# Optimization experiments

Hardware: AMD Instinct MI355X
Metric: run time of the kernel (lower is better)

## Reference

```python
import jax, jax.numpy as jnp
import numpy as np

L, H, NH, DH, FF, V, S, B = 12, 768, 12, 64, 3072, 21128, 512, 8
SEP = 102
LN_EPS = 1e-12


def _ln(x, g, b):
    m = jnp.mean(x, axis=-1, keepdims=True)
    v = jnp.mean(jnp.square(x - m), axis=-1, keepdims=True)
    return (x - m) * jax.lax.rsqrt(v + LN_EPS) * g + b


def setup_inputs() -> dict:
    key = jax.random.key(0)
    ctr = [0]
    def nk():
        ctr[0] += 1
        return jax.random.fold_in(key, ctr[0])
    def p(shape):
        return (0.02 * jax.random.normal(nk(), shape)).astype(jnp.float32)

    input_ids = jax.random.randint(nk(), (B, S), 0, V)
    sep_cols = jax.random.randint(nk(), (B,), 32, 128)
    input_ids = input_ids.at[jnp.arange(B), sep_cols].set(SEP)  # plant [SEP] per row
    labels = jax.random.randint(nk(), (B, S), 0, V)

    return dict(
        input_ids=input_ids, labels=labels,
        word_emb=p((V, H)), pos_emb=p((S, H)), type_emb=p((2, H)),
        emb_ln_g=jnp.ones((H,), jnp.float32), emb_ln_b=jnp.zeros((H,), jnp.float32),
        Wq=p((L, H, H)), bq=jnp.zeros((L, H), jnp.float32),
        Wk=p((L, H, H)), bk=jnp.zeros((L, H), jnp.float32),
        Wv=p((L, H, H)), bv=jnp.zeros((L, H), jnp.float32),
        Wo=p((L, H, H)), bo=jnp.zeros((L, H), jnp.float32),
        ln1_g=jnp.ones((L, H), jnp.float32), ln1_b=jnp.zeros((L, H), jnp.float32),
        Wi=p((L, H, FF)), bi=jnp.zeros((L, FF), jnp.float32),
        Wd=p((L, FF, H)), bd=jnp.zeros((L, H), jnp.float32),
        ln2_g=jnp.ones((L, H), jnp.float32), ln2_b=jnp.zeros((L, H), jnp.float32),
        Wc=p((H, V)), bc=jnp.zeros((V,), jnp.float32),
    )


def reference(input_ids, labels, word_emb, pos_emb, type_emb, emb_ln_g, emb_ln_b,
              Wq, bq, Wk, bk, Wv, bv, Wo, bo, ln1_g, ln1_b,
              Wi, bi, Wd, bd, ln2_g, ln2_b, Wc, bc):
    Bn, Sn = input_ids.shape
    # UniLM prefix-causal mask: bidirectional up to (and incl.) first SEP, causal after
    eq = input_ids == SEP
    sep = jnp.where(eq.any(axis=1), jnp.argmax(eq, axis=1), Sn - 1)        # [B]
    qi = jnp.arange(Sn)[:, None]
    ki = jnp.arange(Sn)[None, :]
    causal = (ki <= qi)                                                    # [S,S]
    prefix = (qi[None] <= sep[:, None, None]) & (ki[None] <= sep[:, None, None])
    mask = (causal[None] | prefix).astype(jnp.float32)                     # [B,S,S]
    bias = ((1.0 - mask) * -1e4)[:, None]                                  # [B,1,S,S]

    # BERT embeddings (token_type all zeros)
    x = word_emb[input_ids] + pos_emb[None, :Sn] + type_emb[0]
    x = _ln(x, emb_ln_g, emb_ln_b)

    scale = 1.0 / np.sqrt(DH).astype(np.float32)
    for l in range(L):
        q = (x @ Wq[l] + bq[l]).reshape(Bn, Sn, NH, DH)
        k = (x @ Wk[l] + bk[l]).reshape(Bn, Sn, NH, DH)
        v = (x @ Wv[l] + bv[l]).reshape(Bn, Sn, NH, DH)
        scores = jnp.einsum('bqhd,bkhd->bhqk', q, k) * scale + bias        # [B,NH,S,S]
        probs = jax.nn.softmax(scores, axis=-1)
        ctx = jnp.einsum('bhqk,bkhd->bqhd', probs, v).reshape(Bn, Sn, H)
        x = _ln(x + ctx @ Wo[l] + bo[l], ln1_g[l], ln1_b[l])
        h = jax.nn.gelu(x @ Wi[l] + bi[l], approximate=False)
        x = _ln(x + h @ Wd[l] + bd[l], ln2_g[l], ln2_b[l])

    logits = x @ Wc + bc                                                   # [B,S,V]
    logp = jax.nn.log_softmax(logits, axis=-1)
    valid = labels >= 0                                                    # ignore_index=-100
    safe = jnp.where(valid, labels, 0)
    nll = -jnp.take_along_axis(logp, safe[..., None], axis=-1)[..., 0]
    loss = jnp.sum(nll * valid) / jnp.maximum(jnp.sum(valid), 1)
    return loss
```

## Files before the change

### kernel.cpp

```cpp
#include <hip/hip_runtime.h>
#include <hip/hip_bf16.h>
#include <cmath>

namespace {

constexpr int LAYERS = 12;
constexpr int H   = 768;
constexpr int NH  = 12;
constexpr int DH  = 64;
constexpr int FF  = 3072;
constexpr int V   = 21128;
constexpr int S   = 512;
constexpr int B   = 8;
constexpr int M   = B * S;
constexpr int SEP = 102;
constexpr int NPAD = 21248;
constexpr int NT64 = NPAD / 64;
constexpr int QKVN = 3 * H;
constexpr size_t MHc = (size_t)M * H;

typedef __attribute__((ext_vector_type(8))) short short8;
typedef __attribute__((ext_vector_type(4))) float floatx4;

__device__ __forceinline__ float geluf(float x) {
  return 0.5f * x * (1.0f + erff(x * 0.70710678118654752f));
}

__device__ __forceinline__ void gload16(const void* g, void* l) {
  __builtin_amdgcn_global_load_lds(
      (const __attribute__((address_space(1))) void*)g,
      (__attribute__((address_space(3))) void*)l, 16, 0, 0);
}

__device__ __forceinline__ unsigned short f2bf(float f) {
  __hip_bfloat16 h = __float2bfloat16(f);
  return *reinterpret_cast<unsigned short*>(&h);
}

__device__ __forceinline__ float block_sum256(float v, float* red) {
  int tid = threadIdx.x;
  red[tid] = v; __syncthreads();
  for (int s2 = 128; s2 > 0; s2 >>= 1) {
    if (tid < s2) red[tid] += red[tid + s2];
    __syncthreads();
  }
  float r = red[0];
  __syncthreads();
  return r;
}

__device__ __forceinline__ float block_max256(float v, float* red) {
  int tid = threadIdx.x;
  red[tid] = v; __syncthreads();
  for (int s2 = 128; s2 > 0; s2 >>= 1) {
    if (tid < s2) red[tid] = fmaxf(red[tid], red[tid + s2]);
    __syncthreads();
  }
  float r = red[0];
  __syncthreads();
  return r;
}

__global__ void sep_kernel(const int* __restrict__ ids, int* __restrict__ sep) {
  int b = blockIdx.x;
  __shared__ int red[256];
  int m = S - 1;
  for (int s = threadIdx.x; s < S; s += 256)
    if (ids[b * S + s] == SEP) m = min(m, s);
  red[threadIdx.x] = m; __syncthreads();
  for (int s2 = 128; s2 > 0; s2 >>= 1) {
    if (threadIdx.x < s2) red[threadIdx.x] = min(red[threadIdx.x], red[threadIdx.x + s2]);
    __syncthreads();
  }
  if (threadIdx.x == 0) sep[b] = red[0];
}

__global__ __launch_bounds__(256) void transpose_kernel(
    const float* __restrict__ W, __hip_bfloat16* __restrict__ Wt,
    int K, int N, int Npad, size_t in_stride, size_t out_stride) {
  const float* Wz = W + (size_t)blockIdx.z * in_stride;
  __hip_bfloat16* Wtz = Wt + (size_t)blockIdx.z * out_stride;
  __shared__ float tile[32][33];
  int k0 = blockIdx.x * 32, n0 = blockIdx.y * 32;
  int tx = threadIdx.x & 31, ty = threadIdx.x >> 5;
  #pragma unroll
  for (int i = 0; i < 4; i++) {
    int kk = k0 + ty + i * 8, nn = n0 + tx;
    tile[ty + i * 8][tx] = (kk < K && nn < N) ? Wz[(size_t)kk * N + nn] : 0.f;
  }
  __syncthreads();
  #pragma unroll
  for (int i = 0; i < 4; i++) {
    int nn = n0 + ty + i * 8, kk = k0 + tx;
    if (nn < Npad && kk < K)
      Wtz[(size_t)nn * K + kk] = __float2bfloat16(tile[tx][ty + i * 8]);
  }
}

__global__ __launch_bounds__(256) void embed_kernel(
    const int* __restrict__ ids, const float* __restrict__ we,
    const float* __restrict__ pe, const float* __restrict__ te,
    const float* __restrict__ g, const float* __restrict__ bta,
    float* __restrict__ x, __hip_bfloat16* __restrict__ xb) {
  __shared__ float red[256];
  int tok = blockIdx.x;
  int s = tok % S;
  int id = ids[tok];
  float vals[3];
  #pragma unroll
  for (int i = 0; i < 3; i++) {
    int hh = threadIdx.x + i * 256;
    vals[i] = we[(size_t)id * H + hh] + pe[(size_t)s * H + hh] + te[hh];
  }
  float mean = block_sum256(vals[0] + vals[1] + vals[2], red) * (1.0f / H);
  float sq = 0.f;
  #pragma unroll
  for (int i = 0; i < 3; i++) { float d = vals[i] - mean; sq += d * d; }
  float var = block_sum256(sq, red) * (1.0f / H);
  float inv = rsqrtf(var + 1e-12f);
  #pragma unroll
  for (int i = 0; i < 3; i++) {
    int hh = threadIdx.x + i * 256;
    float o = (vals[i] - mean) * inv * g[hh] + bta[hh];
    x[(size_t)tok * H + hh] = o;
    xb[(size_t)tok * H + hh] = __float2bfloat16(o);
  }
}

template <int NS>
__global__ __launch_bounds__(256) void add_ln_kernel(
    const float* __restrict__ resid, const float* __restrict__ t,
    const float* __restrict__ g, const float* __restrict__ bta,
    float* __restrict__ out, __hip_bfloat16* __restrict__ outb) {
  __shared__ float red[256];
  int tok = blockIdx.x;
  float vals[3];
  #pragma unroll
  for (int i = 0; i < 3; i++) {
    size_t idx = (size_t)tok * H + threadIdx.x + i * 256;
    float v = resid[idx];
    #pragma unroll
    for (int z = 0; z < NS; z++) v += t[z * MHc + idx];
    vals[i] = v;
  }
  float mean = block_sum256(vals[0] + vals[1] + vals[2], red) * (1.0f / H);
  float sq = 0.f;
  #pragma unroll
  for (int i = 0; i < 3; i++) { float d = vals[i] - mean; sq += d * d; }
  float var = block_sum256(sq, red) * (1.0f / H);
  float inv = rsqrtf(var + 1e-12f);
  #pragma unroll
  for (int i = 0; i < 3; i++) {
    int hh = threadIdx.x + i * 256;
    float o = (vals[i] - mean) * inv * g[hh] + bta[hh];
    out[(size_t)tok * H + hh] = o;
    outb[(size_t)tok * H + hh] = __float2bfloat16(o);
  }
}

template <int K, int N, int EPI, int SPLIT = 1>
__global__ __launch_bounds__(256) void mfma_gemm(
    const short* __restrict__ A, const short* __restrict__ Bt,
    const float* __restrict__ bias,
    float* __restrict__ Cf, __hip_bfloat16* __restrict__ Cb,
    const int* __restrict__ labels, float2* __restrict__ partials,
    float* __restrict__ lablogit,
    __hip_bfloat16* __restrict__ Cb2, __hip_bfloat16* __restrict__ Cb3,
    const float* __restrict__ bias2, const float* __restrict__ bias3) {
  __shared__ __align__(16) short lds_a[128 * 32];
  __shared__ __align__(16) short lds_b[128 * 32];
  const int tid = threadIdx.x, lane = tid & 63, w = tid >> 6;
  const int wm = w >> 1, wn = w & 1;
  const int row0 = blockIdx.y * 128, col0 = blockIdx.x * 128;
  const int g = lane >> 4, c16 = lane & 15;
  const int srow = w * 32 + (lane >> 2);
  const int schunk = lane & 3;
  floatx4 acc[4][4] = {};

  constexpr int Ks = K / SPLIT;
  const int koff = (SPLIT > 1) ? (int)blockIdx.z * Ks : 0;

  for (int k0 = koff; k0 < koff + Ks; k0 += 32) {
    #pragma unroll
    for (int j = 0; j < 2; j++) {
      int m = srow + j * 16;
      int cg = schunk ^ ((m >> 1) & 3);
      gload16(A + (size_t)(row0 + m) * K + (k0 + cg * 8), lds_a + w * 1024 + j * 512);
      gload16(Bt + (size_t)(col0 + m) * K + (k0 + cg * 8), lds_b + w * 1024 + j * 512);
    }
    __syncthreads();
    short8 af[4], bfr[4];
    #pragma unroll
    for (int t = 0; t < 4; t++) {
      int rm = wm * 64 + t * 16 + c16;
      af[t] = *(const short8*)(lds_a + rm * 32 + ((g ^ ((rm >> 1) & 3)) << 3));
      int rn = wn * 64 + t * 16 + c16;
      bfr[t] = *(const short8*)(lds_b + rn * 32 + ((g ^ ((rn >> 1) & 3)) << 3));
    }
    #pragma unroll
    for (int mt = 0; mt < 4; mt++)
      #pragma unroll
      for (int nt = 0; nt < 4; nt++)
        acc[mt][nt] = __builtin_amdgcn_mfma_f32_16x16x32_bf16(af[mt], bfr[nt], acc[mt][nt], 0, 0, 0);
    __syncthreads();
  }

  if constexpr (EPI == 0) {
    float* Cfz = Cf + (size_t)blockIdx.z * ((size_t)M * N);
    #pragma unroll
    for (int mt = 0; mt < 4; mt++)
      #pragma unroll
      for (int r = 0; r < 4; r++) {
        int row = row0 + wm * 64 + mt * 16 + g * 4 + r;
        #pragma unroll
        for (int nt = 0; nt < 4; nt++) {
          int col = col0 + wn * 64 + nt * 16 + c16;
          float bb = (SPLIT == 1 || blockIdx.z == 0) ? bias[col] : 0.f;
          Cfz[(size_t)row * N + col] = acc[mt][nt][r] + bb;
        }
      }
  } else if constexpr (EPI == 1 || EPI == 2) {
    #pragma unroll
    for (int mt = 0; mt < 4; mt++)
      #pragma unroll
      for (int r = 0; r < 4; r++) {
        int row = row0 + wm * 64 + mt * 16 + g * 4 + r;
        #pragma unroll
        for (int nt = 0; nt < 4; nt++) {
          int col = col0 + wn * 64 + nt * 16 + c16;
          float vv = acc[mt][nt][r] + bias[col];
          if constexpr (EPI == 2) vv = geluf(vv);
          Cb[(size_t)row * N + col] = __float2bfloat16(vv);
        }
      }
  } else if constexpr (EPI == 4) {
    unsigned short* vt = (unsigned short*)Cb;
    #pragma unroll
    for (int mt = 0; mt < 4; mt++) {
      int row = row0 + wm * 64 + mt * 16 + g * 4;
      int bb = row >> 9, s0 = row & 511;
      #pragma unroll
      for (int nt = 0; nt < 4; nt++) {
        int col = col0 + wn * 64 + nt * 16 + c16;
        int h = col >> 6, d = col & 63;
        float bcol = bias[col];
        uint2 u;
        unsigned short p0 = f2bf(acc[mt][nt][0] + bcol);
        unsigned short p1 = f2bf(acc[mt][nt][1] + bcol);
        unsigned short p2 = f2bf(acc[mt][nt][2] + bcol);
        unsigned short p3 = f2bf(acc[mt][nt][3] + bcol);
        u.x = (unsigned int)p0 | ((unsigned int)p1 << 16);
        u.y = (unsigned int)p2 | ((unsigned int)p3 << 16);
        *(uint2*)(vt + ((size_t)((bb * NH + h) * DH + d) << 9) + s0) = u;
      }
    }
  } else if constexpr (EPI == 5) {
    const int sect = col0 / H;
    const int lc0 = col0 - sect * H;
    if (sect < 2) {
      __hip_bfloat16* out = (sect == 0) ? Cb : Cb2;
      const float* bptr = (sect == 0) ? bias : bias2;
      #pragma unroll
      for (int mt = 0; mt < 4; mt++)
        #pragma unroll
        for (int r = 0; r < 4; r++) {
          int row = row0 + wm * 64 + mt * 16 + g * 4 + r;
          #pragma unroll
          for (int nt = 0; nt < 4; nt++) {
            int lc = lc0 + wn * 64 + nt * 16 + c16;
            out[(size_t)row * H + lc] = __float2bfloat16(acc[mt][nt][r] + bptr[lc]);
          }
        }
    } else {
      unsigned short* vt = (unsigned short*)Cb3;
      #pragma unroll
      for (int mt = 0; mt < 4; mt++) {
        int row = row0 + wm * 64 + mt * 16 + g * 4;
        int bb = row >> 9, s0 = row & 511;
        #pragma unroll
        for (int nt = 0; nt < 4; nt++) {
          int lc = lc0 + wn * 64 + nt * 16 + c16;
          int h = lc >> 6, d = lc & 63;
          float bcol = bias3[lc];
          uint2 u;
          unsigned short p0 = f2bf(acc[mt][nt][0] + bcol);
          unsigned short p1 = f2bf(acc[mt][nt][1] + bcol);
          unsigned short p2 = f2bf(acc[mt][nt][2] + bcol);
          unsigned short p3 = f2bf(acc[mt][nt][3] + bcol);
          u.x = (unsigned int)p0 | ((unsigned int)p1 << 16);
          u.y = (unsigned int)p2 | ((unsigned int)p3 << 16);
          *(uint2*)(vt + ((size_t)((bb * NH + h) * DH + d) << 9) + s0) = u;
        }
      }
    }
  } else {
    #pragma unroll
    for (int mt = 0; mt < 4; mt++)
      #pragma unroll
      for (int r = 0; r < 4; r++) {
        int row = row0 + wm * 64 + mt * 16 + g * 4 + r;
        int lab = labels[row];
        float vals[4];
        float rmax = -1e30f;
        #pragma unroll
        for (int nt = 0; nt < 4; nt++) {
          int col = col0 + wn * 64 + nt * 16 + c16;
          float vv = (col < V) ? (acc[mt][nt][r] + bias[col]) : -60000.0f;
          vals[nt] = vv;
          rmax = fmaxf(rmax, vv);
          if (col == lab) lablogit[row] = vv;
        }
        #pragma unroll
        for (int d = 1; d < 16; d <<= 1) rmax = fmaxf(rmax, __shfl_xor(rmax, d, 64));
        float se = 0.f;
        #pragma unroll
        for (int nt = 0; nt < 4; nt++) se += __expf(vals[nt] - rmax);
        #pragma unroll
        for (int d = 1; d < 16; d <<= 1) se += __shfl_xor(se, d, 64);
        if (c16 == 0)
          partials[(size_t)row * NT64 + (col0 >> 6) + wn] = make_float2(rmax, se);
      }
  }
}

__global__ __launch_bounds__(256) void flash_attn(
    const short* __restrict__ q, const short* __restrict__ k,
    const short* __restrict__ vt, const int* __restrict__ sep,
    __hip_bfloat16* __restrict__ ctx) {
  constexpr int KT = 128;
  __shared__ __align__(16) short Qs[64 * 64];
  __shared__ __align__(16) short Ks[128 * 64];
  __shared__ __align__(16) short Vts[64 * 128];
  __shared__ __align__(16) short Pb[64 * 136];
  __shared__ __align__(16) float wm4[4][64];
  __shared__ __align__(16) float wl4[4][64];
  __shared__ __align__(16) float m_run[64], l_run[64], alpha_s[64], mnew_s[64];

  const int tid = threadIdx.x, lane = tid & 63, w = tid >> 6;
  const int g = lane >> 4, c16 = lane & 15;
  const int qt0 = blockIdx.x * 64, h = blockIdx.y, b = blockIdx.z;
  const int sepb = sep[b];

  if (tid < 64) { m_run[tid] = -1e30f; l_run[tid] = 0.f; }

  #pragma unroll
  for (int t = 0; t < 2; t++) {
    int id = (w * 2 + t) * 64 + lane;
    int row = id >> 3, slot = id & 7;
    int c = slot ^ (row & 7);
    gload16(q + (size_t)(b * S + qt0 + row) * H + h * DH + c * 8,
            Qs + (w * 2 + t) * 512);
  }

  int niter = (qt0 + 64 + KT - 1) / KT;
  int sepit = (sepb >> 7) + 1;
  if (sepit > niter) niter = sepit;

  floatx4 accO[4] = {};
  short8 qf[4][2];

  for (int it = 0; it < niter; ++it) {
    int kk0 = it * KT;
    __syncthreads();
    #pragma unroll
    for (int t = 0; t < 4; t++) {
      int id = (w * 4 + t) * 64 + lane;
      {
        int row = id >> 3, slot = id & 7, c = slot ^ (row & 7);
        gload16(k + (size_t)(b * S + kk0 + row) * H + h * DH + c * 8,
                Ks + (w * 4 + t) * 512);
      }
      {
        int row = id >> 4, slot = id & 15, c = slot ^ (row & 15);
        gload16(vt + (size_t)((b * NH + h) * DH + row) * S + kk0 + c * 8,
                Vts + (w * 4 + t) * 512);
      }
    }
    __syncthreads();

    if (it == 0) {
      #pragma unroll
      for (int nt = 0; nt < 4; nt++)
        #pragma unroll
        for (int st = 0; st < 2; st++) {
          int qq = nt * 16 + c16;
          int slot = (st * 4 + g) ^ (qq & 7);
          qf[nt][st] = *(const short8*)(Qs + qq * 64 + slot * 8);
        }
    }

    floatx4 accS[2][4] = {};
    #pragma unroll
    for (int st = 0; st < 2; st++) {
      short8 af[2];
      #pragma unroll
      for (int mt = 0; mt < 2; mt++) {
        int kkr = w * 32 + mt * 16 + c16;
        int slot = (st * 4 + g) ^ (kkr & 7);
        af[mt] = *(const short8*)(Ks + kkr * 64 + slot * 8);
      }
      #pragma unroll
      for (int mt = 0; mt < 2; mt++)
        #pragma unroll
        for (int nt = 0; nt < 4; nt++)
          accS[mt][nt] = __builtin_amdgcn_mfma_f32_16x16x32_bf16(
              af[mt], qf[nt][st], accS[mt][nt], 0, 0, 0);
    }

    float sc[2][4][4];
    float pm[4] = {-1e30f, -1e30f, -1e30f, -1e30f};
    #pragma unroll
    for (int mt = 0; mt < 2; mt++)
      #pragma unroll
      for (int nt = 0; nt < 4; nt++)
        #pragma unroll
        for (int r = 0; r < 4; r++) {
          int kkg = kk0 + w * 32 + mt * 16 + g * 4 + r;
          int qg = qt0 + nt * 16 + c16;
          bool allowed = (kkg <= qg) || (qg <= sepb && kkg <= sepb);
          float vv = accS[mt][nt][r] * 0.125f + (allowed ? 0.f : -1e4f);
          sc[mt][nt][r] = vv;
          pm[nt] = fmaxf(pm[nt], vv);
        }
    #pragma unroll
    for (int nt = 0; nt < 4; nt++) {
      pm[nt] = fmaxf(pm[nt], __shfl_xor(pm[nt], 16, 64));
      pm[nt] = fmaxf(pm[nt], __shfl_xor(pm[nt], 32, 64));
    }
    if (lane < 16) {
      #pragma unroll
      for (int nt = 0; nt < 4; nt++) wm4[w][nt * 16 + c16] = pm[nt];
    }
    __syncthreads();
    if (tid < 64) {
      float mit = fmaxf(fmaxf(wm4[0][tid], wm4[1][tid]), fmaxf(wm4[2][tid], wm4[3][tid]));
      float mold = m_run[tid];
      float mnew = fmaxf(mold, mit);
      float al = __expf(mold - mnew);
      m_run[tid] = mnew;
      alpha_s[tid] = al;
      mnew_s[tid] = mnew;
      l_run[tid] *= al;
    }
    __syncthreads();

    float psum[4] = {};
    #pragma unroll
    for (int mt = 0; mt < 2; mt++)
      #pragma unroll
      for (int nt = 0; nt < 4; nt++) {
        int qg = nt * 16 + c16;
        float mn = mnew_s[qg];
        unsigned short pk[4];
        #pragma unroll
        for (int r = 0; r < 4; r++) {
          float p = __expf(sc[mt][nt][r] - mn);
          psum[nt] += p;
          pk[r] = f2bf(p);
        }
        int kb = w * 32 + mt * 16 + g * 4;
        uint2 u;
        u.x = (unsigned int)pk[0] | ((unsigned int)pk[1] << 16);
        u.y = (unsigned int)pk[2] | ((unsigned int)pk[3] << 16);
        *(uint2*)(Pb + qg * 136 + kb) = u;
      }
    #pragma unroll
    for (int nt = 0; nt < 4; nt++) {
      psum[nt] += __shfl_xor(psum[nt], 16, 64);
      psum[nt] += __shfl_xor(psum[nt], 32, 64);
    }
    if (lane < 16) {
      #pragma unroll
      for (int nt = 0; nt < 4; nt++) wl4[w][nt * 16 + c16] = psum[nt];
    }
    {
      float4 a4 = *(const float4*)(alpha_s + w * 16 + g * 4);
      #pragma unroll
      for (int nt = 0; nt < 4; nt++) {
        accO[nt][0] *= a4.x; accO[nt][1] *= a4.y;
        accO[nt][2] *= a4.z; accO[nt][3] *= a4.w;
      }
    }
    __syncthreads();
    if (tid < 64)
      l_run[tid] += wl4[0][tid] + wl4[1][tid] + wl4[2][tid] + wl4[3][tid];

    #pragma unroll
    for (int st = 0; st < 4; st++) {
      short8 pf = *(const short8*)(Pb + (w * 16 + c16) * 136 + st * 32 + g * 8);
      #pragma unroll
      for (int nt = 0; nt < 4; nt++) {
        int d = nt * 16 + c16;
        int slot = (st * 4 + g) ^ (d & 15);
        short8 vf = *(const short8*)(Vts + d * 128 + slot * 8);
        accO[nt] = __builtin_amdgcn_mfma_f32_16x16x32_bf16(pf, vf, accO[nt], 0, 0, 0);
      }
    }
  }

  __syncthreads();
  float4 lv = *(const float4*)(l_run + w * 16 + g * 4);
  float linv[4] = {1.0f / lv.x, 1.0f / lv.y, 1.0f / lv.z, 1.0f / lv.w};
  #pragma unroll
  for (int r = 0; r < 4; r++) {
    int row = b * S + qt0 + w * 16 + g * 4 + r;
    #pragma unroll
    for (int nt = 0; nt < 4; nt++)
      ctx[(size_t)row * H + h * DH + nt * 16 + c16] =
          __float2bfloat16(accO[nt][r] * linv[r]);
  }
}

__global__ __launch_bounds__(256) void loss_kernel(
    const float2* __restrict__ partials, const float* __restrict__ lablogit,
    const int* __restrict__ labels, float* __restrict__ acc) {
  int tok = blockIdx.x;
  if (labels[tok] < 0) return;
  __shared__ float red[256];
  float lm = -1e30f;
  for (int t = threadIdx.x; t < NT64; t += 256)
    lm = fmaxf(lm, partials[(size_t)tok * NT64 + t].x);
  float Mx = block_max256(lm, red);
  float ls = 0.f;
  for (int t = threadIdx.x; t < NT64; t += 256) {
    float2 p = partials[(size_t)tok * NT64 + t];
    ls += p.y * __expf(p.x - Mx);
  }
  float Ssum = block_sum256(ls, red);
  if (threadIdx.x == 0) {
    float nll = (Mx + logf(Ssum)) - lablogit[tok];
    atomicAdd(&acc[0], nll);
    atomicAdd(&acc[1], 1.0f);
  }
}

__global__ void finalize_kernel(const float* __restrict__ acc, float* __restrict__ out) {
  out[0] = acc[0] / fmaxf(acc[1], 1.0f);
}

}

extern "C" void kernel_launch(void* const* d_in, const int* in_sizes, int n_in,
                              void* d_out, int out_size, void* d_ws, size_t ws_size,
                              hipStream_t stream) {
  const int*   input_ids = (const int*)d_in[0];
  const int*   labels    = (const int*)d_in[1];
  const float* word_emb  = (const float*)d_in[2];
  const float* pos_emb   = (const float*)d_in[3];
  const float* type_emb  = (const float*)d_in[4];
  const float* emb_ln_g  = (const float*)d_in[5];
  const float* emb_ln_b  = (const float*)d_in[6];
  const float* Wq = (const float*)d_in[7];
  const float* bq = (const float*)d_in[8];
  const float* Wk = (const float*)d_in[9];
  const float* bk = (const float*)d_in[10];
  const float* Wv = (const float*)d_in[11];
  const float* bv = (const float*)d_in[12];
  const float* Wo = (const float*)d_in[13];
  const float* bo = (const float*)d_in[14];
  const float* ln1_g = (const float*)d_in[15];
  const float* ln1_b = (const float*)d_in[16];
  const float* Wi = (const float*)d_in[17];
  const float* bi = (const float*)d_in[18];
  const float* Wd = (const float*)d_in[19];
  const float* bd = (const float*)d_in[20];
  const float* ln2_g = (const float*)d_in[21];
  const float* ln2_b = (const float*)d_in[22];
  const float* Wc = (const float*)d_in[23];
  const float* bc = (const float*)d_in[24];

  char* base = (char*)d_ws;
  size_t off = 0;
  auto alloc = [&](size_t bytes) -> void* {
    void* p = base + off;
    off = (off + bytes + 255) & ~(size_t)255;
    return p;
  };
  const size_t MH = (size_t)M * H;
  float*          x        = (float*)alloc(MH * 4);
  float*          t2       = (float*)alloc(MH * 4 * 4);
  __hip_bfloat16* xb       = (__hip_bfloat16*)alloc(MH * 2);
  __hip_bfloat16* qb       = (__hip_bfloat16*)alloc(MH * 2);
  __hip_bfloat16* kb       = (__hip_bfloat16*)alloc(MH * 2);
  __hip_bfloat16* vt       = (__hip_bfloat16*)alloc((size_t)B * NH * DH * S * 2);
  __hip_bfloat16* ctxb     = (__hip_bfloat16*)alloc(MH * 2);
  __hip_bfloat16* t1b      = (__hip_bfloat16*)alloc((size_t)M * FF * 2);
  float2*         partials = (float2*)alloc((size_t)M * NT64 * 8);
  float*          lablogit = (float*)alloc((size_t)M * 4);
  float*          acc      = (float*)alloc(2 * 4);
  int*            sep      = (int*)alloc(B * 4);
  __hip_bfloat16* wqkv_t = (__hip_bfloat16*)alloc((size_t)LAYERS * QKVN * H * 2);
  __hip_bfloat16* wo_t = (__hip_bfloat16*)alloc((size_t)LAYERS * H * H * 2);
  __hip_bfloat16* wi_t = (__hip_bfloat16*)alloc((size_t)FF * H * 2);
  __hip_bfloat16* wd_t = (__hip_bfloat16*)alloc((size_t)H * FF * 2);
  __hip_bfloat16* wc_t = (__hip_bfloat16*)alloc((size_t)NPAD * H * 2);

  hipMemsetAsync(acc, 0, 2 * sizeof(float), stream);

  sep_kernel<<<B, 256, 0, stream>>>(input_ids, sep);
  embed_kernel<<<M, 256, 0, stream>>>(input_ids, word_emb, pos_emb, type_emb,
                                      emb_ln_g, emb_ln_b, x, xb);

  {
    dim3 tg(H / 32, H / 32, LAYERS);
    transpose_kernel<<<tg, 256, 0, stream>>>(Wq, wqkv_t, H, H, H,
                                             (size_t)H * H, (size_t)QKVN * H);
    transpose_kernel<<<tg, 256, 0, stream>>>(Wk, wqkv_t + (size_t)H * H, H, H, H,
                                             (size_t)H * H, (size_t)QKVN * H);
    transpose_kernel<<<tg, 256, 0, stream>>>(Wv, wqkv_t + (size_t)2 * H * H, H, H, H,
                                             (size_t)H * H, (size_t)QKVN * H);
    transpose_kernel<<<tg, 256, 0, stream>>>(Wo, wo_t, H, H, H, (size_t)H * H, (size_t)H * H);
    dim3 tgc(H / 32, NPAD / 32, 1);
    transpose_kernel<<<tgc, 256, 0, stream>>>(Wc, wc_t, H, V, NPAD, 0, 0);
  }

  dim3 gQKV(QKVN / 128, M / 128);
  dim3 gO(H / 128, M / 128, 2);
  dim3 gF(FF / 128, M / 128);
  dim3 gD(H / 128, M / 128, 4);
  dim3 gAttn(S / 64, NH, B);

  for (int l = 0; l < LAYERS; l++) {
    transpose_kernel<<<dim3(H / 32, FF / 32, 1), 256, 0, stream>>>(
        Wi + (size_t)l * H * FF, wi_t, H, FF, FF, 0, 0);
    transpose_kernel<<<dim3(FF / 32, H / 32, 1), 256, 0, stream>>>(
        Wd + (size_t)l * FF * H, wd_t, FF, H, H, 0, 0);

    const short* xbs = (const short*)xb;
    mfma_gemm<H, QKVN, 5><<<gQKV, 256, 0, stream>>>(
        xbs, (const short*)(wqkv_t + (size_t)l * QKVN * H), bq + (size_t)l * H,
        nullptr, qb, nullptr, nullptr, nullptr,
        kb, vt, bk + (size_t)l * H, bv + (size_t)l * H);
    flash_attn<<<gAttn, 256, 0, stream>>>(
        (const short*)qb, (const short*)kb, (const short*)vt, sep, ctxb);
    mfma_gemm<H, H, 0, 2><<<gO, 256, 0, stream>>>(
        (const short*)ctxb, (const short*)(wo_t + (size_t)l * H * H), bo + (size_t)l * H,
        t2, nullptr, nullptr, nullptr, nullptr,
        nullptr, nullptr, nullptr, nullptr);
    add_ln_kernel<2><<<M, 256, 0, stream>>>(x, t2, ln1_g + (size_t)l * H,
                                            ln1_b + (size_t)l * H, x, xb);
    mfma_gemm<H, FF, 2><<<gF, 256, 0, stream>>>(
        (const short*)xb, (const short*)wi_t, bi + (size_t)l * FF,
        nullptr, t1b, nullptr, nullptr, nullptr,
        nullptr, nullptr, nullptr, nullptr);
    mfma_gemm<FF, H, 0, 4><<<gD, 256, 0, stream>>>(
        (const short*)t1b, (const short*)wd_t, bd + (size_t)l * H,
        t2, nullptr, nullptr, nullptr, nullptr,
        nullptr, nullptr, nullptr, nullptr);
    add_ln_kernel<4><<<M, 256, 0, stream>>>(x, t2, ln2_g + (size_t)l * H,
                                            ln2_b + (size_t)l * H, x, xb);
  }

  dim3 gV(NPAD / 128, M / 128);
  mfma_gemm<H, NPAD, 3><<<gV, 256, 0, stream>>>(
      (const short*)xb, (const short*)wc_t, bc,
      nullptr, nullptr, labels, partials, lablogit,
      nullptr, nullptr, nullptr, nullptr);
  loss_kernel<<<M, 256, 0, stream>>>(partials, lablogit, labels, acc);
  finalize_kernel<<<1, 1, 0, stream>>>(acc, (float*)d_out);
}
```

Baseline: 3.172 ms.

## Deepen GEMM K-tile to 64 and swizzle block order for vocab GEMM

The MFMA GEMM now stages 64-wide K slices in LDS with an 8-way XOR swizzle, which halves the number of barrier pairs per K step and doubles MFMA work per sync. The vocabulary projection GEMM also remaps block IDs so that consecutive workgroups are spread across the grid, aiming for better L2 reuse of the weight and activation tiles. It also removes the unused EPI 4 transposed-V epilogue. The larger LDS footprint (32KB per block) may reduce occupancy.

Result: slower. 3.417 ms (+7.8%).

```diff
diff --git a/kernel.cpp b/kernel.cpp
--- a/kernel.cpp
+++ b/kernel.cpp
@@ -158,7 +158,7 @@
   }
 }
 
-template <int K, int N, int EPI, int SPLIT = 1>
+template <int K, int N, int EPI, int SPLIT = 1, bool SWZ = false>
 __global__ __launch_bounds__(256) void mfma_gemm(
     const short* __restrict__ A, const short* __restrict__ Bt,
     const float* __restrict__ bias,
@@ -167,41 +167,56 @@
     float* __restrict__ lablogit,
     __hip_bfloat16* __restrict__ Cb2, __hip_bfloat16* __restrict__ Cb3,
     const float* __restrict__ bias2, const float* __restrict__ bias3) {
-  __shared__ __align__(16) short lds_a[128 * 32];
-  __shared__ __align__(16) short lds_b[128 * 32];
+  __shared__ __align__(16) short lds_a[128 * 64];
+  __shared__ __align__(16) short lds_b[128 * 64];
   const int tid = threadIdx.x, lane = tid & 63, w = tid >> 6;
   const int wm = w >> 1, wn = w & 1;
-  const int row0 = blockIdx.y * 128, col0 = blockIdx.x * 128;
   const int g = lane >> 4, c16 = lane & 15;
-  const int srow = w * 32 + (lane >> 2);
-  const int schunk = lane & 3;
+
+  int bx = blockIdx.x, by = blockIdx.y;
+  if constexpr (SWZ) {
+    constexpr int NBX = N / 128;
+    constexpr int GR = M / 128;
+    constexpr int NWG = NBX * GR;
+    static_assert(NWG % 8 == 0, "swizzle needs nwg %% 8 == 0");
+    int lid = by * NBX + bx;
+    int j = (lid & 7) * (NWG >> 3) + (lid >> 3);
+    bx = j / GR; by = j % GR;
+  }
+  const int row0 = by * 128, col0 = bx * 128;
+
   floatx4 acc[4][4] = {};
 
   constexpr int Ks = K / SPLIT;
   const int koff = (SPLIT > 1) ? (int)blockIdx.z * Ks : 0;
 
-  for (int k0 = koff; k0 < koff + Ks; k0 += 32) {
-    #pragma unroll
-    for (int j = 0; j < 2; j++) {
-      int m = srow + j * 16;
-      int cg = schunk ^ ((m >> 1) & 3);
-      gload16(A + (size_t)(row0 + m) * K + (k0 + cg * 8), lds_a + w * 1024 + j * 512);
-      gload16(Bt + (size_t)(col0 + m) * K + (k0 + cg * 8), lds_b + w * 1024 + j * 512);
-    }
-    __syncthreads();
-    short8 af[4], bfr[4];
-    #pragma unroll
-    for (int t = 0; t < 4; t++) {
-      int rm = wm * 64 + t * 16 + c16;
-      af[t] = *(const short8*)(lds_a + rm * 32 + ((g ^ ((rm >> 1) & 3)) << 3));
-      int rn = wn * 64 + t * 16 + c16;
-      bfr[t] = *(const short8*)(lds_b + rn * 32 + ((g ^ ((rn >> 1) & 3)) << 3));
-    }
-    #pragma unroll
-    for (int mt = 0; mt < 4; mt++)
-      #pragma unroll
-      for (int nt = 0; nt < 4; nt++)
-        acc[mt][nt] = __builtin_amdgcn_mfma_f32_16x16x32_bf16(af[mt], bfr[nt], acc[mt][nt], 0, 0, 0);
+  for (int k0 = koff; k0 < koff + Ks; k0 += 64) {
+    #pragma unroll
+    for (int j = 0; j < 4; j++) {
+      int row = w * 32 + j * 8 + (lane >> 3);
+      int cg = (lane & 7) ^ (row & 7);
+      gload16(A + (size_t)(row0 + row) * K + (k0 + cg * 8),
+              lds_a + w * 2048 + j * 512 + lane * 8);
+      gload16(Bt + (size_t)(col0 + row) * K + (k0 + cg * 8),
+              lds_b + w * 2048 + j * 512 + lane * 8);
+    }
+    __syncthreads();
+    #pragma unroll
+    for (int ks = 0; ks < 2; ks++) {
+      short8 af[4], bfr[4];
+      #pragma unroll
+      for (int t = 0; t < 4; t++) {
+        int rm = wm * 64 + t * 16 + c16;
+        af[t] = *(const short8*)(lds_a + rm * 64 + (((ks * 4 + g) ^ (rm & 7)) << 3));
+        int rn = wn * 64 + t * 16 + c16;
+        bfr[t] = *(const short8*)(lds_b + rn * 64 + (((ks * 4 + g) ^ (rn & 7)) << 3));
+      }
+      #pragma unroll
+      for (int mt = 0; mt < 4; mt++)
+        #pragma unroll
+        for (int nt = 0; nt < 4; nt++)
+          acc[mt][nt] = __builtin_amdgcn_mfma_f32_16x16x32_bf16(af[mt], bfr[nt], acc[mt][nt], 0, 0, 0);
+    }
     __syncthreads();
   }
 
@@ -233,27 +248,6 @@
           Cb[(size_t)row * N + col] = __float2bfloat16(vv);
         }
       }
-  } else if constexpr (EPI == 4) {
-    unsigned short* vt = (unsigned short*)Cb;
-    #pragma unroll
-    for (int mt = 0; mt < 4; mt++) {
-      int row = row0 + wm * 64 + mt * 16 + g * 4;
-      int bb = row >> 9, s0 = row & 511;
-      #pragma unroll
-      for (int nt = 0; nt < 4; nt++) {
-        int col = col0 + wn * 64 + nt * 16 + c16;
-        int h = col >> 6, d = col & 63;
-        float bcol = bias[col];
-        uint2 u;
-        unsigned short p0 = f2bf(acc[mt][nt][0] + bcol);
-        unsigned short p1 = f2bf(acc[mt][nt][1] + bcol);
-        unsigned short p2 = f2bf(acc[mt][nt][2] + bcol);
-        unsigned short p3 = f2bf(acc[mt][nt][3] + bcol);
-        u.x = (unsigned int)p0 | ((unsigned int)p1 << 16);
-        u.y = (unsigned int)p2 | ((unsigned int)p3 << 16);
-        *(uint2*)(vt + ((size_t)((bb * NH + h) * DH + d) << 9) + s0) = u;
-      }
-    }
   } else if constexpr (EPI == 5) {
     const int sect = col0 / H;
     const int lc0 = col0 - sect * H;
@@ -652,7 +646,7 @@
   }
 
   dim3 gV(NPAD / 128, M / 128);
-  mfma_gemm<H, NPAD, 3><<<gV, 256, 0, stream>>>(
+  mfma_gemm<H, NPAD, 3, 1, true><<<gV, 256, 0, stream>>>(
       (const short*)xb, (const short*)wc_t, bc,
       nullptr, nullptr, labels, partials, lablogit,
       nullptr, nullptr, nullptr, nullptr);
```
